# Kernel tuning notes

Measured on AMD Instinct MI355X. Metric: run time of the kernel, lower is better.

## Reference

```python
import jax, jax.numpy as jnp
import numpy as np

EPS_BN = 1e-5
EPS_LN = 1e-5
B_, CIN, COUT, H_, W_ = 8, 64, 128, 64, 64
DSTATE, DCONV, EXPAND = 16, 4, 2
DINNER = EXPAND * COUT            # 256
DTRANK = (COUT + 15) // 16        # 8


def setup_inputs() -> dict:
    key = jax.random.key(0)
    ks = jax.random.split(key, 24)
    g = lambda i, shape, s=0.02: jax.random.normal(ks[i], shape, jnp.float32) * s
    inp = {}
    inp["x"] = jax.random.normal(ks[0], (B_, CIN, H_, W_), jnp.float32)
    # conv-bn-relu x2
    inp["conv1_w"] = g(1, (COUT, CIN, 3, 3), 0.05)
    inp["conv1_b"] = jnp.zeros((COUT,), jnp.float32)
    inp["bn1_g"] = jnp.ones((COUT,), jnp.float32)
    inp["bn1_b"] = jnp.zeros((COUT,), jnp.float32)
    inp["bn1_m"] = g(2, (COUT,), 0.1)
    inp["bn1_v"] = jnp.ones((COUT,), jnp.float32)
    inp["conv2_w"] = g(3, (COUT, COUT, 3, 3), 0.05)
    inp["conv2_b"] = jnp.zeros((COUT,), jnp.float32)
    inp["bn2_g"] = jnp.ones((COUT,), jnp.float32)
    inp["bn2_b"] = jnp.zeros((COUT,), jnp.float32)
    inp["bn2_m"] = g(4, (COUT,), 0.1)
    inp["bn2_v"] = jnp.ones((COUT,), jnp.float32)
    # Mamba params (mamba_ssm defaults: projections bias-free except dt_proj)
    inp["in_proj_w"] = g(5, (2 * DINNER, COUT))
    inp["conv1d_w"] = g(6, (DINNER, 1, DCONV), 0.1)   # depthwise
    inp["conv1d_b"] = jnp.zeros((DINNER,), jnp.float32)
    inp["x_proj_w"] = g(7, (DTRANK + 2 * DSTATE, DINNER))
    inp["dt_proj_w"] = g(8, (DINNER, DTRANK), 0.1)
    inp["dt_proj_b"] = g(9, (DINNER,), 0.5)
    # S4D-real init: A = -[1..d_state] per channel
    A = jnp.tile(jnp.arange(1, DSTATE + 1, dtype=jnp.float32)[None, :], (DINNER, 1))
    inp["A_log"] = jnp.log(A)
    inp["D"] = jnp.ones((DINNER,), jnp.float32)
    inp["out_proj_w"] = g(10, (COUT, DINNER))
    inp["ln_g"] = jnp.ones((COUT,), jnp.float32)
    inp["ln_b"] = jnp.zeros((COUT,), jnp.float32)
    return inp


def _conv3x3(x, w, b):
    y = jax.lax.conv_general_dilated(x, w, (1, 1), ((1, 1), (1, 1)),
                                     dimension_numbers=("NCHW", "OIHW", "NCHW"))
    return y + b[None, :, None, None]


def _bn_eval(x, g, b, m, v):
    inv = jax.lax.rsqrt(v + EPS_BN)
    return (x - m[None, :, None, None]) * (g * inv)[None, :, None, None] + b[None, :, None, None]


def _mamba(x_flat, in_proj_w, conv1d_w, conv1d_b, x_proj_w, dt_proj_w, dt_proj_b, A_log, D, out_proj_w):
    # x_flat: (B, L, C)
    Bsz, L, _ = x_flat.shape
    xz = jnp.einsum("blc,ec->ble", x_flat, in_proj_w)          # (B, L, 2*di)
    xm, z = jnp.split(xz, 2, axis=-1)                           # each (B, L, di)
    # causal depthwise conv1d over time
    xt = jnp.transpose(xm, (0, 2, 1))                           # (B, di, L)
    xt = jax.lax.conv_general_dilated(xt, conv1d_w, (1,), ((DCONV - 1, 0),),
                                      dimension_numbers=("NCH", "OIH", "NCH"),
                                      feature_group_count=DINNER)
    xt = xt + conv1d_b[None, :, None]
    x_ssm = jax.nn.silu(jnp.transpose(xt, (0, 2, 1)))           # (B, L, di)
    xdb = jnp.einsum("bld,ed->ble", x_ssm, x_proj_w)            # (B, L, dt_rank+2*ds)
    dt_r = xdb[..., :DTRANK]
    Bm = xdb[..., DTRANK:DTRANK + DSTATE]                       # (B, L, ds)
    Cm = xdb[..., DTRANK + DSTATE:]                             # (B, L, ds)
    dt = jax.nn.softplus(jnp.einsum("blr,dr->bld", dt_r, dt_proj_w) + dt_proj_b)
    A = -jnp.exp(A_log)                                         # (di, ds)

    def step(h, inp):
        dt_t, B_t, C_t, x_t = inp                               # (B,di) (B,ds) (B,ds) (B,di)
        dA = jnp.exp(dt_t[:, :, None] * A)                      # (B, di, ds)
        h = dA * h + (dt_t * x_t)[:, :, None] * B_t[:, None, :]
        y = jnp.einsum("bds,bs->bd", h, C_t)
        return h, y

    xs = (jnp.swapaxes(dt, 0, 1), jnp.swapaxes(Bm, 0, 1),
          jnp.swapaxes(Cm, 0, 1), jnp.swapaxes(x_ssm, 0, 1))
    h0 = jnp.zeros((Bsz, DINNER, DSTATE), jnp.float32)
    _, ys = jax.lax.scan(step, h0, xs)                          # (L, B, di)
    y = jnp.swapaxes(ys, 0, 1) + D * x_ssm
    y = y * jax.nn.silu(z)
    return jnp.einsum("bld,od->blo", y, out_proj_w)             # (B, L, C)


def reference(x, conv1_w, conv1_b, bn1_g, bn1_b, bn1_m, bn1_v,
              conv2_w, conv2_b, bn2_g, bn2_b, bn2_m, bn2_v,
              in_proj_w, conv1d_w, conv1d_b, x_proj_w, dt_proj_w, dt_proj_b,
              A_log, D, out_proj_w, ln_g, ln_b):
    h = jax.nn.relu(_bn_eval(_conv3x3(x, conv1_w, conv1_b), bn1_g, bn1_b, bn1_m, bn1_v))
    h = jax.nn.relu(_bn_eval(_conv3x3(h, conv2_w, conv2_b), bn2_g, bn2_b, bn2_m, bn2_v))
    Bsz, C, Hh, Ww = h.shape
    seq = jnp.transpose(h, (0, 2, 3, 1)).reshape(Bsz, Hh * Ww, C)
    seq = _mamba(seq, in_proj_w, conv1d_w, conv1d_b, x_proj_w,
                 dt_proj_w, dt_proj_b, A_log, D, out_proj_w)
    # LayerNorm over channels
    mu = jnp.mean(seq, axis=-1, keepdims=True)
    var = jnp.mean(jnp.square(seq - mu), axis=-1, keepdims=True)
    seq = (seq - mu) * jax.lax.rsqrt(var + EPS_LN) * ln_g + ln_b
    return jnp.transpose(seq.reshape(Bsz, Hh, Ww, C), (0, 3, 1, 2))
```

## Files before the change

### kernel.cpp

```cpp
#include <hip/hip_runtime.h>
#include <hip/hip_bf16.h>


typedef __attribute__((ext_vector_type(8))) short bf16x8;
typedef __attribute__((ext_vector_type(4))) float f32x4;

#define DEV __device__ __forceinline__

constexpr float LOG2E = 1.44269504088896f;

DEV float siluf(float v) {
  return v * __builtin_amdgcn_rcpf(1.f + __expf(-v));
}

DEV unsigned short f2bf(float f) {
  __hip_bfloat16 h = __float2bfloat16(f);
  return *reinterpret_cast<unsigned short*>(&h);
}

DEV float bf2f(unsigned short u) {
  unsigned int x = (unsigned int)u << 16;
  return __builtin_bit_cast(float, x);
}

DEV void gll16(const void* g, void* l) {
  __builtin_amdgcn_global_load_lds(
      (const __attribute__((address_space(1))) void*)g,
      (__attribute__((address_space(3))) void*)l, 16, 0, 0);
}

constexpr int NC = 256;
constexpr int CL = 16;

DEV void zero_border(unsigned short* buf, int CI, int tid0, int nthreads) {
  for (int w = tid0; w < 8 * 260; w += nthreads) {
    int b = w / 260, e = w % 260;
    int y, x;
    if (e < 132) { y = (e < 66) ? 0 : 65; x = (e < 66) ? e : e - 66; }
    else { int e2 = e - 132; y = 1 + (e2 >> 1); x = (e2 & 1) ? 65 : 0; }
    uint4* p = reinterpret_cast<uint4*>(buf + ((size_t)((b * 66 + y) * 66 + x)) * CI);
    for (int k = 0; k < CI / 8; ++k) p[k] = uint4{0u, 0u, 0u, 0u};
  }
}

__global__ __launch_bounds__(256) void prologue(
    const float* __restrict__ X, unsigned short* __restrict__ Xb,
    const float* __restrict__ conv1_w, const float* __restrict__ conv2_w,
    const float* __restrict__ in_proj_w, const float* __restrict__ out_proj_w,
    const float* __restrict__ x_proj_w, const float* __restrict__ A_log,
    unsigned short* __restrict__ wb1, unsigned short* __restrict__ wb2,
    unsigned short* __restrict__ win, unsigned short* __restrict__ wout,
    unsigned short* __restrict__ xpwb, float* __restrict__ An2f,
    unsigned short* __restrict__ h1p)
{
  __shared__ float t[64][65];
  const int blk = blockIdx.x;
  const int tid = threadIdx.x;
  if (blk < 512) {
    const int b = blk >> 6, y = blk & 63;
    for (int i = tid; i < 4096; i += 256) {
      int c = i >> 6, xx = i & 63;
      t[c][xx] = X[(((size_t)b * 64 + c) * 64 + y) * 64 + xx];
    }
    __syncthreads();
    for (int i = tid; i < 4096; i += 256) {
      int xx = i >> 6, c = i & 63;
      Xb[(((size_t)(b * 66 + y + 1) * 66) + xx + 1) * 64 + c] = f2bf(t[c][xx]);
    }
  } else if (blk < 1904) {
    int idx = (blk - 512) * 256 + tid;
    if (idx < 73728) {
      int co = idx / 576, r = idx % 576, tp = r >> 6, ci = r & 63;
      wb1[idx] = f2bf(conv1_w[((size_t)co * 64 + ci) * 9 + tp]);
    } else if (idx < 221184) {
      int i = idx - 73728;
      int co = i / 1152, r = i % 1152, tp = r >> 7, ci = r & 127;
      wb2[i] = f2bf(conv2_w[((size_t)co * 128 + ci) * 9 + tp]);
    } else if (idx < 286720) {
      int i = idx - 221184; win[i] = f2bf(in_proj_w[i]);
    } else if (idx < 319488) {
      int i = idx - 286720; wout[i] = f2bf(out_proj_w[i]);
    } else if (idx < 352256) {
      int i = idx - 319488; int r = i >> 8, c = i & 255;
      xpwb[i] = (r < 40) ? f2bf(x_proj_w[r * 256 + c]) : (unsigned short)0;
    } else if (idx < 356352) {
      int i = idx - 352256;
      An2f[i] = -__expf(A_log[i]) * LOG2E;
    }
  } else {
    int tid0 = (blk - 1904) * 256 + tid;
    zero_border(Xb, 64, tid0, 16 * 256);
    zero_border(h1p, 128, tid0, 16 * 256);
  }
}

template<int CI, int PADOUT>
__global__ __launch_bounds__(256) void conv_mfma(
    const unsigned short* __restrict__ Xp,
    const unsigned short* __restrict__ Wb,
    const float* __restrict__ bc,
    const float* __restrict__ bg, const float* __restrict__ bb,
    const float* __restrict__ bm, const float* __restrict__ bv,
    unsigned short* __restrict__ Y)
{
  constexpr int KC  = 3 * CI / 64;
  constexpr int NCH = 3 * KC;
  __shared__ bf16x8 ldsA[2][512];

  const int lane = threadIdx.x & 63;
  const int wid  = threadIdx.x >> 6;
  const int n0 = wid * 32;
  const int y = blockIdx.x, b = blockIdx.y;
  const int lr = lane & 15, kq = lane >> 4, lk = kq * 8;

  auto stage = [&](int buf, int c) {
    const int dy = c / KC, kc = c - dy * KC;
    const unsigned short* g = Xp
        + (size_t)((b * 66 + y + dy) * 66) * CI
        + (size_t)lane * CI + kc * 64 + wid * 16;
    gll16(g,     &ldsA[buf][(wid * 2) * 64]);
    gll16(g + 8, &ldsA[buf][(wid * 2 + 1) * 64]);
  };

  f32x4 acc[4][2];
  #pragma unroll
  for (int i = 0; i < 4; ++i)
    #pragma unroll
    for (int j = 0; j < 2; ++j) acc[i][j] = f32x4{0.f, 0.f, 0.f, 0.f};

  stage(0, 0);
  __syncthreads();

  #pragma unroll
  for (int c = 0; c < NCH; ++c) {
    if (c + 1 < NCH) stage((c + 1) & 1, c + 1);
    const int dy = c / KC, kc = c - dy * KC;
    bf16x8 bw[2][2];
    #pragma unroll
    for (int t = 0; t < 2; ++t)
      #pragma unroll
      for (int nf = 0; nf < 2; ++nf)
        bw[t][nf] = *reinterpret_cast<const bf16x8*>(
            Wb + (size_t)(n0 + nf * 16 + lr) * (9 * CI)
               + dy * 3 * CI + kc * 64 + t * 32 + lk);
    const bf16x8* Ab = ldsA[c & 1];
    #pragma unroll
    for (int t = 0; t < 2; ++t)
      #pragma unroll
      for (int mf = 0; mf < 4; ++mf) {
        bf16x8 afr = Ab[(t * 4 + kq) * 64 + mf * 16 + lr];
        #pragma unroll
        for (int nf = 0; nf < 2; ++nf)
          acc[mf][nf] = __builtin_amdgcn_mfma_f32_16x16x32_bf16(
              afr, bw[t][nf], acc[mf][nf], 0, 0, 0);
      }
    __syncthreads();
  }

  #pragma unroll
  for (int nf = 0; nf < 2; ++nf) {
    int n = n0 + nf * 16 + lr;
    float aS = bg[n] * rsqrtf(bv[n] + 1e-5f);
    float aB = (bc[n] - bm[n]) * aS + bb[n];
    #pragma unroll
    for (int mf = 0; mf < 4; ++mf)
      #pragma unroll
      for (int i = 0; i < 4; ++i) {
        int m = mf * 16 + kq * 4 + i;
        float v = fmaxf(acc[mf][nf][i] * aS + aB, 0.f);
        if (PADOUT)
          Y[((size_t)(b * 66 + y + 1) * 66 + m + 1) * 128 + n] = f2bf(v);
        else
          Y[((size_t)(b * 4096 + y * 64 + m)) * 128 + n] = f2bf(v);
      }
  }
}

__global__ __launch_bounds__(256) void inproj_fused(
    const unsigned short* __restrict__ A,
    const unsigned short* __restrict__ Wn,
    const float* __restrict__ c1w,
    const float* __restrict__ c1b,
    unsigned short* __restrict__ xsu,
    unsigned short* __restrict__ zbu)
{
  constexpr int KDIM = 128;
  __shared__ bf16x8 ldsA[2][512];
  __shared__ unsigned short xmt[67][136];
  __shared__ unsigned short s3[3][128];
  __shared__ float cw[128][4];
  __shared__ float cbias[128];

  const int tid = threadIdx.x;
  const int lane = tid & 63, wid = tid >> 6;
  const int m0 = blockIdx.x * 64;
  const int by = blockIdx.y;
  const int n0 = by * 128 + wid * 32;
  const int lr = lane & 15, kq = lane >> 4, lk = kq * 8;
  const int l0 = m0 & 4095;

  if (by < 2) {
    for (int w = tid; w < 384; w += 256) {
      int j = w >> 7, k = w & 127;
      s3[j][k] = (l0 == 0) ? (unsigned short)0
                           : A[(size_t)(m0 - 3 + j) * 128 + k];
    }
    if (tid < 128) {
      int dd = by * 128 + tid;
      cw[tid][0] = c1w[dd * 4 + 0]; cw[tid][1] = c1w[dd * 4 + 1];
      cw[tid][2] = c1w[dd * 4 + 2]; cw[tid][3] = c1w[dd * 4 + 3];
      cbias[tid] = c1b[dd];
    }
  }

  bf16x8 bw[2][2][2];
  #pragma unroll
  for (int c = 0; c < 2; ++c)
    #pragma unroll
    for (int t = 0; t < 2; ++t)
      #pragma unroll
      for (int nf = 0; nf < 2; ++nf)
        bw[c][t][nf] = *reinterpret_cast<const bf16x8*>(
            Wn + (size_t)(n0 + nf * 16 + lr) * KDIM + c * 64 + t * 32 + lk);

  auto stage = [&](int buf, int c) {
    const unsigned short* g = A + (size_t)(m0 + lane) * KDIM + c * 64 + wid * 16;
    gll16(g,     &ldsA[buf][(wid * 2) * 64]);
    gll16(g + 8, &ldsA[buf][(wid * 2 + 1) * 64]);
  };

  f32x4 acc[4][2];
  #pragma unroll
  for (int i = 0; i < 4; ++i)
    #pragma unroll
    for (int j = 0; j < 2; ++j) acc[i][j] = f32x4{0.f, 0.f, 0.f, 0.f};

  stage(0, 0);
  __syncthreads();

  #pragma unroll
  for (int c = 0; c < 2; ++c) {
    if (c + 1 < 2) stage((c + 1) & 1, c + 1);
    const bf16x8* Ab = ldsA[c & 1];
    #pragma unroll
    for (int t = 0; t < 2; ++t)
      #pragma unroll
      for (int mf = 0; mf < 4; ++mf) {
        bf16x8 afr = Ab[(t * 4 + kq) * 64 + mf * 16 + lr];
        #pragma unroll
        for (int nf = 0; nf < 2; ++nf)
          acc[mf][nf] = __builtin_amdgcn_mfma_f32_16x16x32_bf16(
              afr, bw[c][t][nf], acc[mf][nf], 0, 0, 0);
      }
    __syncthreads();
  }

  if (by >= 2) {
    #pragma unroll
    for (int nf = 0; nf < 2; ++nf) {
      int n = n0 + nf * 16 + lr - 256;
      #pragma unroll
      for (int mf = 0; mf < 4; ++mf)
        #pragma unroll
        for (int i = 0; i < 4; ++i)
          zbu[(size_t)(m0 + mf * 16 + kq * 4 + i) * 256 + n] =
              f2bf(siluf(acc[mf][nf][i]));
    }
    return;
  }

  #pragma unroll
  for (int nf = 0; nf < 2; ++nf) {
    int ch = wid * 32 + nf * 16 + lr;
    #pragma unroll
    for (int mf = 0; mf < 4; ++mf)
      #pragma unroll
      for (int i = 0; i < 4; ++i)
        xmt[3 + mf * 16 + kq * 4 + i][ch] = f2bf(acc[mf][nf][i]);
  }
  __syncthreads();

  for (int w = tid; w < 384; w += 256) {
    int j = w >> 7, ch = w & 127;
    float a = 0.f;
    if (l0 != 0) {
      const unsigned short* wr = Wn + (size_t)(by * 128 + ch) * 128;
      #pragma unroll 4
      for (int k0 = 0; k0 < 128; k0 += 8) {
        bf16x8 wv = *reinterpret_cast<const bf16x8*>(wr + k0);
        #pragma unroll
        for (int k = 0; k < 8; ++k)
          a = fmaf(bf2f(s3[j][k0 + k]), bf2f((unsigned short)wv[k]), a);
      }
    }
    xmt[j][ch] = f2bf(a);
  }
  __syncthreads();

  const int tg = tid & 15, ch8 = tid >> 4;
  float wr8[8][4], br8[8];
  #pragma unroll
  for (int k = 0; k < 8; ++k) {
    int chl = ch8 * 8 + k;
    wr8[k][0] = cw[chl][0]; wr8[k][1] = cw[chl][1];
    wr8[k][2] = cw[chl][2]; wr8[k][3] = cw[chl][3];
    br8[k] = cbias[chl];
  }
  #pragma unroll
  for (int tk = 0; tk < 4; ++tk) {
    int m = tg * 4 + tk;
    float o[8];
    #pragma unroll
    for (int k = 0; k < 8; ++k) o[k] = br8[k];
    #pragma unroll
    for (int j = 0; j < 4; ++j) {
      uint4 xv = *reinterpret_cast<const uint4*>(&xmt[m + j][ch8 * 8]);
      const unsigned short* xs = reinterpret_cast<const unsigned short*>(&xv);
      #pragma unroll
      for (int k = 0; k < 8; ++k)
        o[k] = fmaf(bf2f(xs[k]), wr8[k][j], o[k]);
    }
    unsigned int pk[4];
    #pragma unroll
    for (int k = 0; k < 4; ++k) {
      unsigned short lo = f2bf(siluf(o[2 * k]));
      unsigned short hi = f2bf(siluf(o[2 * k + 1]));
      pk[k] = (unsigned int)lo | ((unsigned int)hi << 16);
    }
    *reinterpret_cast<uint4*>(
        &xsu[(size_t)(m0 + m) * 256 + by * 128 + ch8 * 8]) =
        *reinterpret_cast<uint4*>(pk);
  }
}

__global__ __launch_bounds__(256) void outproj_ln(
    const unsigned short* __restrict__ A,
    const unsigned short* __restrict__ Wn,
    const float* __restrict__ lg, const float* __restrict__ lb,
    float* __restrict__ out)
{
  constexpr int KDIM = 256;
  constexpr int NCH = KDIM / 64;
  __shared__ bf16x8 ldsA[2][512];
  __shared__ float buf[64][129];

  const int lane = threadIdx.x & 63;
  const int wid  = threadIdx.x >> 6;
  const int m0 = blockIdx.x * 64;
  const int n0 = wid * 32;
  const int lr = lane & 15, kq = lane >> 4, lk = kq * 8;

  bf16x8 bw[NCH][2][2];
  #pragma unroll
  for (int c = 0; c < NCH; ++c)
    #pragma unroll
    for (int t = 0; t < 2; ++t)
      #pragma unroll
      for (int nf = 0; nf < 2; ++nf)
        bw[c][t][nf] = *reinterpret_cast<const bf16x8*>(
            Wn + (size_t)(n0 + nf * 16 + lr) * KDIM + c * 64 + t * 32 + lk);

  auto stage = [&](int buf2, int c) {
    const unsigned short* g = A + (size_t)(m0 + lane) * KDIM + c * 64 + wid * 16;
    gll16(g,     &ldsA[buf2][(wid * 2) * 64]);
    gll16(g + 8, &ldsA[buf2][(wid * 2 + 1) * 64]);
  };

  f32x4 acc[4][2];
  #pragma unroll
  for (int i = 0; i < 4; ++i)
    #pragma unroll
    for (int j = 0; j < 2; ++j) acc[i][j] = f32x4{0.f, 0.f, 0.f, 0.f};

  stage(0, 0);
  __syncthreads();

  #pragma unroll
  for (int c = 0; c < NCH; ++c) {
    if (c + 1 < NCH) stage((c + 1) & 1, c + 1);
    const bf16x8* Ab = ldsA[c & 1];
    #pragma unroll
    for (int t = 0; t < 2; ++t)
      #pragma unroll
      for (int mf = 0; mf < 4; ++mf) {
        bf16x8 afr = Ab[(t * 4 + kq) * 64 + mf * 16 + lr];
        #pragma unroll
        for (int nf = 0; nf < 2; ++nf)
          acc[mf][nf] = __builtin_amdgcn_mfma_f32_16x16x32_bf16(
              afr, bw[c][t][nf], acc[mf][nf], 0, 0, 0);
      }
    __syncthreads();
  }

  #pragma unroll
  for (int nf = 0; nf < 2; ++nf) {
    int n = n0 + nf * 16 + lr;
    #pragma unroll
    for (int mf = 0; mf < 4; ++mf)
      #pragma unroll
      for (int i = 0; i < 4; ++i)
        buf[mf * 16 + kq * 4 + i][n] = acc[mf][nf][i];
  }
  __syncthreads();

  const int tid = threadIdx.x;
  const int tt = tid >> 2, q = tid & 3;
  float s = 0.f, sq = 0.f;
  #pragma unroll
  for (int i = 0; i < 32; ++i) {
    float v = buf[tt][q * 32 + i];
    s += v; sq += v * v;
  }
  s  += __shfl_xor(s, 1);  s  += __shfl_xor(s, 2);
  sq += __shfl_xor(sq, 1); sq += __shfl_xor(sq, 2);
  float mu = s * (1.f / 128.f);
  float var = sq * (1.f / 128.f) - mu * mu;
  float rstd = rsqrtf(fmaxf(var, 0.f) + 1e-5f);
  #pragma unroll
  for (int i = 0; i < 32; ++i) {
    int c = q * 32 + i;
    buf[tt][c] = (buf[tt][c] - mu) * rstd * lg[c] + lb[c];
  }
  __syncthreads();

  const int bb = m0 >> 12, l0 = m0 & 4095;
  for (int idx = tid; idx < 64 * 128; idx += 256) {
    int c = idx >> 6, t2 = idx & 63;
    out[((size_t)bb * 128 + c) * 4096 + l0 + t2] = buf[t2][c];
  }
}

__global__ __launch_bounds__(256) void scan_pass1(
    const unsigned short* __restrict__ xssm,
    const unsigned short* __restrict__ xpw,
    const float* __restrict__ dtw, const float* __restrict__ dtb,
    const float* __restrict__ An2f,
    unsigned short* __restrict__ Qb, float* __restrict__ S)
{
  __shared__ __align__(16) float sh[CL][40];
  const int c = blockIdx.x, b = blockIdx.y;
  const int d = threadIdx.x;
  const int lane = threadIdx.x & 63, wid = threadIdx.x >> 6;
  if (wid < 3) {
    const int col0 = wid * 16;
    const int plr = lane & 15, plk = (lane >> 4) * 8;
    f32x4 pacc = f32x4{0.f, 0.f, 0.f, 0.f};
    const unsigned short* Xrow =
        xssm + ((size_t)b * 4096 + (size_t)c * CL + plr) * 256;
    const unsigned short* Wrow = xpw + (size_t)(col0 + plr) * 256;
    #pragma unroll
    for (int k0 = 0; k0 < 256; k0 += 32) {
      bf16x8 af = *reinterpret_cast<const bf16x8*>(Xrow + k0 + plk);
      bf16x8 bf = *reinterpret_cast<const bf16x8*>(Wrow + k0 + plk);
      pacc = __builtin_amdgcn_mfma_f32_16x16x32_bf16(af, bf, pacc, 0, 0, 0);
    }
    int col = col0 + (lane & 15);
    if (col < 40) {
      #pragma unroll
      for (int i = 0; i < 4; ++i)
        sh[(lane >> 4) * 4 + i][col] = pacc[i];
    }
  }
  float4 w0 = *reinterpret_cast<const float4*>(&dtw[d * 8]);
  float4 w1 = *reinterpret_cast<const float4*>(&dtw[d * 8 + 4]);
  const float bdt = dtb[d];
  float An2[16], h[16];
  {
    const f32x4* a2 = reinterpret_cast<const f32x4*>(&An2f[d * 16]);
    #pragma unroll
    for (int q = 0; q < 4; ++q) {
      f32x4 v = a2[q];
      An2[q * 4 + 0] = v[0]; An2[q * 4 + 1] = v[1];
      An2[q * 4 + 2] = v[2]; An2[q * 4 + 3] = v[3];
    }
  }
  #pragma unroll
  for (int s = 0; s < 16; ++s) h[s] = 0.f;
  __syncthreads();

  float sdt = 0.f;
  const size_t xbase = ((size_t)b * 4096 + (size_t)c * CL) * 256 + d;
  unsigned short xu = xssm[xbase];
  for (int l = 0; l < CL; ++l) {
    unsigned short xun = (l + 1 < CL) ? xssm[xbase + (size_t)(l + 1) * 256]
                                      : (unsigned short)0;
    const float4* row = reinterpret_cast<const float4*>(sh[l]);
    float4 r0 = row[0], r1 = row[1];
    float acc = bdt;
    acc = fmaf(r0.x, w0.x, acc); acc = fmaf(r0.y, w0.y, acc);
    acc = fmaf(r0.z, w0.z, acc); acc = fmaf(r0.w, w0.w, acc);
    acc = fmaf(r1.x, w1.x, acc); acc = fmaf(r1.y, w1.y, acc);
    acc = fmaf(r1.z, w1.z, acc); acc = fmaf(r1.w, w1.w, acc);
    float dt = (acc > 20.f) ? acc : __logf(1.f + __expf(acc));
    sdt += dt;
    float dtx = dt * bf2f(xu);
    #pragma unroll
    for (int q = 0; q < 4; ++q) {
      float4 Bq = row[2 + q];
      float bb4[4] = {Bq.x, Bq.y, Bq.z, Bq.w};
      #pragma unroll
      for (int j = 0; j < 4; ++j) {
        int s = q * 4 + j;
        float dA = __builtin_amdgcn_exp2f(dt * An2[s]);
        h[s] = fmaf(dA, h[s], dtx * bb4[j]);
      }
    }
    xu = xun;
  }
  unsigned int pk[8];
  #pragma unroll
  for (int k = 0; k < 8; ++k)
    pk[k] = (unsigned int)f2bf(h[2 * k]) | ((unsigned int)f2bf(h[2 * k + 1]) << 16);
  uint4* qp = reinterpret_cast<uint4*>(
      &Qb[(((size_t)b * NC + c) * 256 + d) * 16]);
  qp[0] = *reinterpret_cast<uint4*>(pk);
  qp[1] = *reinterpret_cast<uint4*>(pk + 4);
  S[((size_t)b * NC + c) * 256 + d] = sdt;
}

__global__ __launch_bounds__(256) void scan_combine(
    unsigned short* __restrict__ Qb, const float* __restrict__ S,
    const float* __restrict__ An2f)
{
  int g = blockIdx.x * 256 + threadIdx.x;
  int b = g >> 12, d = (g >> 4) & 255, s = g & 15;
  float An2 = An2f[d * 16 + s];
  const size_t qbase = (size_t)b * NC * 4096 + d * 16 + s;
  const size_t sbase = (size_t)b * NC * 256 + d;
  float h = 0.f;
  unsigned short qn = Qb[qbase];
  float sn = S[sbase];
  for (int c = 0; c < NC; ++c) {
    float q = bf2f(qn), sd = sn;
    if (c + 1 < NC) {
      qn = Qb[qbase + (size_t)(c + 1) * 4096];
      sn = S[sbase + (size_t)(c + 1) * 256];
    }
    Qb[qbase + (size_t)c * 4096] = f2bf(h);
    h = fmaf(__builtin_amdgcn_exp2f(An2 * sd), h, q);
  }
}

__global__ __launch_bounds__(256) void scan_pass2(
    const unsigned short* __restrict__ xssm,
    const unsigned short* __restrict__ xpw,
    const unsigned short* __restrict__ zb,
    const float* __restrict__ dtw, const float* __restrict__ dtb,
    const float* __restrict__ An2f, const float* __restrict__ Dp,
    const unsigned short* __restrict__ Hstart, unsigned short* __restrict__ ybf)
{
  __shared__ __align__(16) float sh[CL][40];
  const int c = blockIdx.x, b = blockIdx.y;
  const int d = threadIdx.x;
  const int lane = threadIdx.x & 63, wid = threadIdx.x >> 6;
  if (wid < 3) {
    const int col0 = wid * 16;
    const int plr = lane & 15, plk = (lane >> 4) * 8;
    f32x4 pacc = f32x4{0.f, 0.f, 0.f, 0.f};
    const unsigned short* Xrow =
        xssm + ((size_t)b * 4096 + (size_t)c * CL + plr) * 256;
    const unsigned short* Wrow = xpw + (size_t)(col0 + plr) * 256;
    #pragma unroll
    for (int k0 = 0; k0 < 256; k0 += 32) {
      bf16x8 af = *reinterpret_cast<const bf16x8*>(Xrow + k0 + plk);
      bf16x8 bf = *reinterpret_cast<const bf16x8*>(Wrow + k0 + plk);
      pacc = __builtin_amdgcn_mfma_f32_16x16x32_bf16(af, bf, pacc, 0, 0, 0);
    }
    int col = col0 + (lane & 15);
    if (col < 40) {
      #pragma unroll
      for (int i = 0; i < 4; ++i)
        sh[(lane >> 4) * 4 + i][col] = pacc[i];
    }
  }
  float4 w0 = *reinterpret_cast<const float4*>(&dtw[d * 8]);
  float4 w1 = *reinterpret_cast<const float4*>(&dtw[d * 8 + 4]);
  const float bdt = dtb[d];
  const float Dd = Dp[d];
  float An2[16], h[16];
  {
    const f32x4* a2 = reinterpret_cast<const f32x4*>(&An2f[d * 16]);
    #pragma unroll
    for (int q = 0; q < 4; ++q) {
      f32x4 v = a2[q];
      An2[q * 4 + 0] = v[0]; An2[q * 4 + 1] = v[1];
      An2[q * 4 + 2] = v[2]; An2[q * 4 + 3] = v[3];
    }
  }
  {
    const uint4* hp = reinterpret_cast<const uint4*>(
        &Hstart[(((size_t)b * NC + c) * 256 + d) * 16]);
    uint4 h0 = hp[0], h1 = hp[1];
    const unsigned short* hs = reinterpret_cast<const unsigned short*>(&h0);
    #pragma unroll
    for (int s = 0; s < 8; ++s) h[s] = bf2f(hs[s]);
    const unsigned short* hs2 = reinterpret_cast<const unsigned short*>(&h1);
    #pragma unroll
    for (int s = 0; s < 8; ++s) h[8 + s] = bf2f(hs2[s]);
  }
  __syncthreads();

  const size_t xbase = ((size_t)b * 4096 + (size_t)c * CL) * 256 + d;
  unsigned short xu = xssm[xbase], zu = zb[xbase];
  for (int l = 0; l < CL; ++l) {
    unsigned short xun = 0, zun = 0;
    if (l + 1 < CL) {
      xun = xssm[xbase + (size_t)(l + 1) * 256];
      zun = zb[xbase + (size_t)(l + 1) * 256];
    }
    const float4* row = reinterpret_cast<const float4*>(sh[l]);
    float4 r0 = row[0], r1 = row[1];
    float acc = bdt;
    acc = fmaf(r0.x, w0.x, acc); acc = fmaf(r0.y, w0.y, acc);
    acc = fmaf(r0.z, w0.z, acc); acc = fmaf(r0.w, w0.w, acc);
    acc = fmaf(r1.x, w1.x, acc); acc = fmaf(r1.y, w1.y, acc);
    acc = fmaf(r1.z, w1.z, acc); acc = fmaf(r1.w, w1.w, acc);
    float dt = (acc > 20.f) ? acc : __logf(1.f + __expf(acc));
    float xv = bf2f(xu);
    float dtx = dt * xv;
    float yq[4] = {0.f, 0.f, 0.f, 0.f};
    #pragma unroll
    for (int q = 0; q < 4; ++q) {
      float4 Bq = row[2 + q], Cq = row[6 + q];
      float bb4[4] = {Bq.x, Bq.y, Bq.z, Bq.w};
      float cc4[4] = {Cq.x, Cq.y, Cq.z, Cq.w};
      #pragma unroll
      for (int j = 0; j < 4; ++j) {
        int s = q * 4 + j;
        float dA = __builtin_amdgcn_exp2f(dt * An2[s]);
        h[s] = fmaf(dA, h[s], dtx * bb4[j]);
        yq[q] = fmaf(h[s], cc4[j], yq[q]);
      }
    }
    float y = (yq[0] + yq[1]) + (yq[2] + yq[3]);
    y = (y + Dd * xv) * bf2f(zu);
    ybf[xbase + (size_t)l * 256] = f2bf(y);
    xu = xun; zu = zun;
  }
}

extern "C" void kernel_launch(void* const* d_in, const int* in_sizes, int n_in,
                              void* d_out, int out_size, void* d_ws, size_t ws_size,
                              hipStream_t stream) {
  const float* x        = (const float*)d_in[0];
  const float* conv1_w  = (const float*)d_in[1];
  const float* conv1_b  = (const float*)d_in[2];
  const float* bn1_g    = (const float*)d_in[3];
  const float* bn1_b    = (const float*)d_in[4];
  const float* bn1_m    = (const float*)d_in[5];
  const float* bn1_v    = (const float*)d_in[6];
  const float* conv2_w  = (const float*)d_in[7];
  const float* conv2_b  = (const float*)d_in[8];
  const float* bn2_g    = (const float*)d_in[9];
  const float* bn2_b    = (const float*)d_in[10];
  const float* bn2_m    = (const float*)d_in[11];
  const float* bn2_v    = (const float*)d_in[12];
  const float* in_proj_w  = (const float*)d_in[13];
  const float* conv1d_w   = (const float*)d_in[14];
  const float* conv1d_b   = (const float*)d_in[15];
  const float* x_proj_w   = (const float*)d_in[16];
  const float* dt_proj_w  = (const float*)d_in[17];
  const float* dt_proj_b  = (const float*)d_in[18];
  const float* A_log      = (const float*)d_in[19];
  const float* Dp         = (const float*)d_in[20];
  const float* out_proj_w = (const float*)d_in[21];
  const float* ln_g       = (const float*)d_in[22];
  const float* ln_b       = (const float*)d_in[23];
  float* out = (float*)d_out;

  float* ws_f = (float*)d_ws;
  unsigned short* xbp  = (unsigned short*)ws_f;
  unsigned short* ybf  = (unsigned short*)ws_f;
  float*          Sbuf = ws_f + 5505024;
  unsigned short* zbu  = (unsigned short*)(ws_f + 8388608);
  unsigned short* xsu  = (unsigned short*)(ws_f + 12582912);
  unsigned short* h1p  = (unsigned short*)(ws_f + 16777216);
  unsigned short* seqb = (unsigned short*)(ws_f + 19007488);
  unsigned short* Qb   = (unsigned short*)(ws_f + 16777216);
  unsigned short* wb1  = (unsigned short*)(ws_f + 25165824);
  unsigned short* wb2  = (unsigned short*)(ws_f + 25202688);
  unsigned short* win  = (unsigned short*)(ws_f + 25276416);
  unsigned short* wout = (unsigned short*)(ws_f + 25309184);
  unsigned short* xpwb = (unsigned short*)(ws_f + 25325568);
  float*          An2f = ws_f + 25341952;

  prologue<<<1920, 256, 0, stream>>>(
      x, xbp, conv1_w, conv2_w, in_proj_w, out_proj_w, x_proj_w, A_log,
      wb1, wb2, win, wout, xpwb, An2f, h1p);

  conv_mfma<64, 1><<<dim3(64, 8), 256, 0, stream>>>(
      xbp, wb1, conv1_b, bn1_g, bn1_b, bn1_m, bn1_v, h1p);
  conv_mfma<128, 0><<<dim3(64, 8), 256, 0, stream>>>(
      h1p, wb2, conv2_b, bn2_g, bn2_b, bn2_m, bn2_v, seqb);

  inproj_fused<<<dim3(512, 4), 256, 0, stream>>>(
      seqb, win, conv1d_w, conv1d_b, xsu, zbu);

  scan_pass1<<<dim3(NC, 8), 256, 0, stream>>>(
      xsu, xpwb, dt_proj_w, dt_proj_b, An2f, Qb, Sbuf);
  scan_combine<<<128, 256, 0, stream>>>(Qb, Sbuf, An2f);
  scan_pass2<<<dim3(NC, 8), 256, 0, stream>>>(
      xsu, xpwb, zbu, dt_proj_w, dt_proj_b, An2f, Dp, Qb, ybf);

  outproj_ln<<<512, 256, 0, stream>>>(ybf, wout, ln_g, ln_b, out);
}
```

Baseline: 212.6 us.

## Compute decay powers by repeated multiply, reuse x_proj output, deepen combine prefetch

When A_log follows the S4D pattern (A_s proportional to s+1), the scan computes one exp2 per step and derives the other decay factors by repeated multiplication, with a runtime check and a general fallback. pass1 stores its x_proj (dt/B/C) results to workspace so pass2 loads them instead of recomputing the MFMA projection. scan_combine prefetches 8 chunks ahead to hide latency. The changes trade transcendental work and redundant matmuls for extra global traffic and slightly different rounding.

```diff
diff --git a/kernel.cpp b/kernel.cpp
--- a/kernel.cpp
+++ b/kernel.cpp
@@ -435,7 +435,8 @@
     const unsigned short* __restrict__ xpw,
     const float* __restrict__ dtw, const float* __restrict__ dtb,
     const float* __restrict__ An2f,
-    unsigned short* __restrict__ Qb, float* __restrict__ S)
+    unsigned short* __restrict__ Qb, float* __restrict__ S,
+    float* __restrict__ xdb)
 {
   __shared__ __align__(16) float sh[CL][40];
   const int c = blockIdx.x, b = blockIdx.y;
@@ -474,9 +475,20 @@
       An2[q * 4 + 2] = v[2]; An2[q * 4 + 3] = v[3];
     }
   }
+  const float An2_0 = An2[0];
+  bool usePow = true;
+  #pragma unroll
+  for (int s = 1; s < 16; ++s)
+    usePow = usePow &&
+        (fabsf(An2[s] - (float)(s + 1) * An2_0) <= 1e-4f * fabsf(An2[s]));
   #pragma unroll
   for (int s = 0; s < 16; ++s) h[s] = 0.f;
   __syncthreads();
+
+  if (d < CL * 10) {
+    reinterpret_cast<float4*>(&xdb[((size_t)b * 4096 + (size_t)c * CL) * 40])[d] =
+        reinterpret_cast<const float4*>(&sh[0][0])[d];
+  }
 
   float sdt = 0.f;
   const size_t xbase = ((size_t)b * 4096 + (size_t)c * CL) * 256 + d;
@@ -494,15 +506,31 @@
     float dt = (acc > 20.f) ? acc : __logf(1.f + __expf(acc));
     sdt += dt;
     float dtx = dt * bf2f(xu);
-    #pragma unroll
-    for (int q = 0; q < 4; ++q) {
-      float4 Bq = row[2 + q];
-      float bb4[4] = {Bq.x, Bq.y, Bq.z, Bq.w};
-      #pragma unroll
-      for (int j = 0; j < 4; ++j) {
-        int s = q * 4 + j;
-        float dA = __builtin_amdgcn_exp2f(dt * An2[s]);
-        h[s] = fmaf(dA, h[s], dtx * bb4[j]);
+    if (usePow) {
+      float r = __builtin_amdgcn_exp2f(dt * An2_0);
+      float da = 1.f;
+      #pragma unroll
+      for (int q = 0; q < 4; ++q) {
+        float4 Bq = row[2 + q];
+        float bb4[4] = {Bq.x, Bq.y, Bq.z, Bq.w};
+        #pragma unroll
+        for (int j = 0; j < 4; ++j) {
+          int s = q * 4 + j;
+          da *= r;
+          h[s] = fmaf(da, h[s], dtx * bb4[j]);
+        }
+      }
+    } else {
+      #pragma unroll
+      for (int q = 0; q < 4; ++q) {
+        float4 Bq = row[2 + q];
+        float bb4[4] = {Bq.x, Bq.y, Bq.z, Bq.w};
+        #pragma unroll
+        for (int j = 0; j < 4; ++j) {
+          int s = q * 4 + j;
+          float dA = __builtin_amdgcn_exp2f(dt * An2[s]);
+          h[s] = fmaf(dA, h[s], dtx * bb4[j]);
+        }
       }
     }
     xu = xun;
@@ -522,28 +550,38 @@
     unsigned short* __restrict__ Qb, const float* __restrict__ S,
     const float* __restrict__ An2f)
 {
+  constexpr int PF = 8;
   int g = blockIdx.x * 256 + threadIdx.x;
   int b = g >> 12, d = (g >> 4) & 255, s = g & 15;
   float An2 = An2f[d * 16 + s];
   const size_t qbase = (size_t)b * NC * 4096 + d * 16 + s;
   const size_t sbase = (size_t)b * NC * 256 + d;
+  unsigned short qv[PF];
+  float sv[PF];
+  #pragma unroll
+  for (int i = 0; i < PF; ++i) {
+    qv[i] = Qb[qbase + (size_t)i * 4096];
+    sv[i] = S[sbase + (size_t)i * 256];
+  }
   float h = 0.f;
-  unsigned short qn = Qb[qbase];
-  float sn = S[sbase];
-  for (int c = 0; c < NC; ++c) {
-    float q = bf2f(qn), sd = sn;
-    if (c + 1 < NC) {
-      qn = Qb[qbase + (size_t)(c + 1) * 4096];
-      sn = S[sbase + (size_t)(c + 1) * 256];
-    }
-    Qb[qbase + (size_t)c * 4096] = f2bf(h);
-    h = fmaf(__builtin_amdgcn_exp2f(An2 * sd), h, q);
+  for (int c0 = 0; c0 < NC; c0 += PF) {
+    #pragma unroll
+    for (int i = 0; i < PF; ++i) {
+      int c = c0 + i;
+      float q = bf2f(qv[i]), sd = sv[i];
+      if (c + PF < NC) {
+        qv[i] = Qb[qbase + (size_t)(c + PF) * 4096];
+        sv[i] = S[sbase + (size_t)(c + PF) * 256];
+      }
+      Qb[qbase + (size_t)c * 4096] = f2bf(h);
+      h = fmaf(__builtin_amdgcn_exp2f(An2 * sd), h, q);
+    }
   }
 }
 
 __global__ __launch_bounds__(256) void scan_pass2(
     const unsigned short* __restrict__ xssm,
-    const unsigned short* __restrict__ xpw,
+    const float* __restrict__ xdb,
     const unsigned short* __restrict__ zb,
     const float* __restrict__ dtw, const float* __restrict__ dtb,
     const float* __restrict__ An2f, const float* __restrict__ Dp,
@@ -552,26 +590,10 @@
   __shared__ __align__(16) float sh[CL][40];
   const int c = blockIdx.x, b = blockIdx.y;
   const int d = threadIdx.x;
-  const int lane = threadIdx.x & 63, wid = threadIdx.x >> 6;
-  if (wid < 3) {
-    const int col0 = wid * 16;
-    const int plr = lane & 15, plk = (lane >> 4) * 8;
-    f32x4 pacc = f32x4{0.f, 0.f, 0.f, 0.f};
-    const unsigned short* Xrow =
-        xssm + ((size_t)b * 4096 + (size_t)c * CL + plr) * 256;
-    const unsigned short* Wrow = xpw + (size_t)(col0 + plr) * 256;
-    #pragma unroll
-    for (int k0 = 0; k0 < 256; k0 += 32) {
-      bf16x8 af = *reinterpret_cast<const bf16x8*>(Xrow + k0 + plk);
-      bf16x8 bf = *reinterpret_cast<const bf16x8*>(Wrow + k0 + plk);
-      pacc = __builtin_amdgcn_mfma_f32_16x16x32_bf16(af, bf, pacc, 0, 0, 0);
-    }
-    int col = col0 + (lane & 15);
-    if (col < 40) {
-      #pragma unroll
-      for (int i = 0; i < 4; ++i)
-        sh[(lane >> 4) * 4 + i][col] = pacc[i];
-    }
+  if (d < CL * 10) {
+    reinterpret_cast<float4*>(&sh[0][0])[d] =
+        reinterpret_cast<const float4*>(
+            &xdb[((size_t)b * 4096 + (size_t)c * CL) * 40])[d];
   }
   float4 w0 = *reinterpret_cast<const float4*>(&dtw[d * 8]);
   float4 w1 = *reinterpret_cast<const float4*>(&dtw[d * 8 + 4]);
@@ -587,6 +609,12 @@
       An2[q * 4 + 2] = v[2]; An2[q * 4 + 3] = v[3];
     }
   }
+  const float An2_0 = An2[0];
+  bool usePow = true;
+  #pragma unroll
+  for (int s = 1; s < 16; ++s)
+    usePow = usePow &&
+        (fabsf(An2[s] - (float)(s + 1) * An2_0) <= 1e-4f * fabsf(An2[s]));
   {
     const uint4* hp = reinterpret_cast<const uint4*>(
         &Hstart[(((size_t)b * NC + c) * 256 + d) * 16]);
@@ -619,17 +647,35 @@
     float xv = bf2f(xu);
     float dtx = dt * xv;
     float yq[4] = {0.f, 0.f, 0.f, 0.f};
-    #pragma unroll
-    for (int q = 0; q < 4; ++q) {
-      float4 Bq = row[2 + q], Cq = row[6 + q];
-      float bb4[4] = {Bq.x, Bq.y, Bq.z, Bq.w};
-      float cc4[4] = {Cq.x, Cq.y, Cq.z, Cq.w};
-      #pragma unroll
-      for (int j = 0; j < 4; ++j) {
-        int s = q * 4 + j;
-        float dA = __builtin_amdgcn_exp2f(dt * An2[s]);
-        h[s] = fmaf(dA, h[s], dtx * bb4[j]);
-        yq[q] = fmaf(h[s], cc4[j], yq[q]);
+    if (usePow) {
+      float r = __builtin_amdgcn_exp2f(dt * An2_0);
+      float da = 1.f;
+      #pragma unroll
+      for (int q = 0; q < 4; ++q) {
+        float4 Bq = row[2 + q], Cq = row[6 + q];
+        float bb4[4] = {Bq.x, Bq.y, Bq.z, Bq.w};
+        float cc4[4] = {Cq.x, Cq.y, Cq.z, Cq.w};
+        #pragma unroll
+        for (int j = 0; j < 4; ++j) {
+          int s = q * 4 + j;
+          da *= r;
+          h[s] = fmaf(da, h[s], dtx * bb4[j]);
+          yq[q] = fmaf(h[s], cc4[j], yq[q]);
+        }
+      }
+    } else {
+      #pragma unroll
+      for (int q = 0; q < 4; ++q) {
+        float4 Bq = row[2 + q], Cq = row[6 + q];
+        float bb4[4] = {Bq.x, Bq.y, Bq.z, Bq.w};
+        float cc4[4] = {Cq.x, Cq.y, Cq.z, Cq.w};
+        #pragma unroll
+        for (int j = 0; j < 4; ++j) {
+          int s = q * 4 + j;
+          float dA = __builtin_amdgcn_exp2f(dt * An2[s]);
+          h[s] = fmaf(dA, h[s], dtx * bb4[j]);
+          yq[q] = fmaf(h[s], cc4[j], yq[q]);
+        }
       }
     }
     float y = (yq[0] + yq[1]) + (yq[2] + yq[3]);
@@ -671,6 +717,7 @@
   float* ws_f = (float*)d_ws;
   unsigned short* xbp  = (unsigned short*)ws_f;
   unsigned short* ybf  = (unsigned short*)ws_f;
+  float*          xdb  = ws_f + 4194304;
   float*          Sbuf = ws_f + 5505024;
   unsigned short* zbu  = (unsigned short*)(ws_f + 8388608);
   unsigned short* xsu  = (unsigned short*)(ws_f + 12582912);
@@ -697,10 +744,10 @@
       seqb, win, conv1d_w, conv1d_b, xsu, zbu);
 
   scan_pass1<<<dim3(NC, 8), 256, 0, stream>>>(
-      xsu, xpwb, dt_proj_w, dt_proj_b, An2f, Qb, Sbuf);
+      xsu, xpwb, dt_proj_w, dt_proj_b, An2f, Qb, Sbuf, xdb);
   scan_combine<<<128, 256, 0, stream>>>(Qb, Sbuf, An2f);
   scan_pass2<<<dim3(NC, 8), 256, 0, stream>>>(
-      xsu, xpwb, zbu, dt_proj_w, dt_proj_b, An2f, Dp, Qb, ybf);
+      xsu, xdb, zbu, dt_proj_w, dt_proj_b, An2f, Dp, Qb, ybf);
 
   outproj_ln<<<512, 256, 0, stream>>>(ybf, wout, ln_g, ln_b, out);
 }
```

Result: slower. 253.3 us (+19.1%).
